# Performance work log

Measured on AMD Instinct MI355X. Metric: run time of the kernel, lower is better.

Reference implementation:

```python
import jax, jax.numpy as jnp
import numpy as np

INPUT_SIZE = 128
HIDDEN = 256
EPS = 1e-5  # PyTorch BatchNorm1d default


def setup_inputs() -> dict:
    key = jax.random.key(0)
    k1, k2, k3 = jax.random.split(key, 3)
    B, S = 128, 1024
    x = jax.random.normal(k1, (B, S, INPUT_SIZE), dtype=jnp.float32)
    fan_in = INPUT_SIZE + HIDDEN
    bound = 1.0 / np.sqrt(fan_in)
    # Linear(input+hidden -> 4*hidden); stored transposed for x @ W
    W = jax.random.uniform(k2, (fan_in, 4 * HIDDEN), minval=-bound, maxval=bound, dtype=jnp.float32)
    b = jax.random.uniform(k3, (4 * HIDDEN,), minval=-bound, maxval=bound, dtype=jnp.float32)
    gamma = jnp.ones((4, HIDDEN), dtype=jnp.float32)   # per-gate BN weight
    beta = jnp.zeros((4, HIDDEN), dtype=jnp.float32)   # per-gate BN bias
    return {"x": x, "W": W, "b": b, "gamma": gamma, "beta": beta}


def reference(x, W, b, gamma, beta):
    B, S, _ = x.shape
    H = HIDDEN

    def step(carry, x_t):
        hx, cx = carry
        g = jnp.concatenate([x_t, hx], axis=1) @ W + b          # [B, 4H]
        g = g.reshape(B, 4, H)
        # BatchNorm1d (training mode): batch statistics per gate/feature
        mean = g.mean(axis=0)                                   # [4, H]
        var = jnp.mean((g - mean) ** 2, axis=0)                 # biased var
        gn = (g - mean) * jax.lax.rsqrt(var + EPS) * gamma + beta
        i = jax.nn.sigmoid(gn[:, 0])
        f = jax.nn.sigmoid(gn[:, 1])
        c = jnp.tanh(gn[:, 2])
        o = jax.nn.sigmoid(gn[:, 3])
        cy = f * cx + i * c
        hy = o * jnp.tanh(cy)
        return (hy, cy), hy

    h0 = jnp.zeros((B, H), dtype=x.dtype)
    c0 = jnp.zeros((B, H), dtype=x.dtype)
    (hy, cy), outs = jax.lax.scan(step, (h0, c0), jnp.swapaxes(x, 0, 1))
    outputs = jnp.swapaxes(outs, 0, 1)                          # [B, S, H]
    return outputs, hy, cy
```

## Files before the change

kernel.cpp:

```cpp
#include <hip/hip_runtime.h>

#define BATCH 128
#define SEQ   1024
#define INSZ  128
#define HID   256
#define NBLK  32
#define NTHR  512
#define FPB   8
#define EPSV  1e-5f
#define SLAB  1032

typedef __attribute__((ext_vector_type(4))) float f32x4;
typedef __attribute__((ext_vector_type(8))) short short8;
typedef __attribute__((ext_vector_type(4))) unsigned u32x4;
typedef unsigned long long u64;
typedef unsigned u32;

__device__ __forceinline__ unsigned short f2bf(float f) {
  unsigned u = __builtin_bit_cast(unsigned, f);
  u += 0x7FFFu + ((u >> 16) & 1u);
  return (unsigned short)(u >> 16);
}
__device__ __forceinline__ short8 xcvt(float4 f0, float4 f1) {
  u32 a, b, c, d2;
  asm("v_cvt_pk_bf16_f32 %0, %1, %2" : "=v"(a)  : "v"(f0.x), "v"(f0.y));
  asm("v_cvt_pk_bf16_f32 %0, %1, %2" : "=v"(b)  : "v"(f0.z), "v"(f0.w));
  asm("v_cvt_pk_bf16_f32 %0, %1, %2" : "=v"(c)  : "v"(f1.x), "v"(f1.y));
  asm("v_cvt_pk_bf16_f32 %0, %1, %2" : "=v"(d2) : "v"(f1.z), "v"(f1.w));
  u32x4 t = {a, b, c, d2};
  return __builtin_bit_cast(short8, t);
}

__launch_bounds__(NTHR)
__global__ void bnlstm_kernel(const float* __restrict__ x,
                              const float* __restrict__ W,
                              const float* __restrict__ gamma,
                              const float* __restrict__ beta,
                              float* __restrict__ out,
                              unsigned short* __restrict__ hbuf,
                              u32* __restrict__ flags) {
  __shared__ __attribute__((aligned(16))) unsigned short Zs[32 * SLAB];
  __shared__ float red1[2][8][32];
  __shared__ float red2[2][8][32];
  __shared__ float waveTr[8][16][17];
  __shared__ __attribute__((aligned(16))) unsigned short hpack[8][16][8];

  const int tid   = threadIdx.x;
  const int bid   = blockIdx.x;
  const int lane  = tid & 63;
  const int wid   = tid >> 6;
  const int col16 = lane & 15;
  const int kg    = lane >> 4;
  const int d     = col16 & 3;
  const int q     = col16 >> 2;
  const int arow  = wid * 16 + col16;
  const int brow  = wid * 16 + kg * 4 + d;
  const int xb    = tid & 127;
  const int gb    = tid >> 7;

  short8 wf[2][12];
  for (int cg = 0; cg < 2; ++cg) {
    const int c32 = cg * 16 + col16;
    const int wcol = (c32 & 3) * HID + bid * FPB + (c32 >> 2);
    for (int kt = 0; kt < 12; ++kt) {
      short8 v;
      for (int e = 0; e < 8; ++e)
        v[e] = (short)f2bf(W[(kt * 32 + kg * 8 + e) * 1024 + wcol]);
      wf[cg][kt] = v;
    }
  }
  float gam = 0.f, bet = 0.f;
  if (lane < 32) {
    gam = gamma[(lane & 3) * HID + bid * FPB + (lane >> 2)];
    bet = beta [(lane & 3) * HID + bid * FPB + (lane >> 2)];
  }

  float cst[2] = {0.f, 0.f};
  float hnv[2];

  const float* xbase = x + (size_t)arow * (SEQ * INSZ) + kg * 8;
  float4 xv[8];
  #pragma unroll
  for (int kt = 0; kt < 4; ++kt) {
    xv[2 * kt]     = *(const float4*)(xbase + kt * 32);
    xv[2 * kt + 1] = *(const float4*)(xbase + kt * 32 + 4);
  }

  for (int t = 0; t < SEQ; ++t) {
    const int pR = t & 1;
    f32x4 acc0 = {0.f, 0.f, 0.f, 0.f}, acc1 = {0.f, 0.f, 0.f, 0.f};

    #pragma unroll
    for (int kt = 0; kt < 4; ++kt) {
      short8 ax = xcvt(xv[2 * kt], xv[2 * kt + 1]);
      acc0 = __builtin_amdgcn_mfma_f32_16x16x32_bf16(ax, wf[0][kt], acc0, 0, 0, 0);
      acc1 = __builtin_amdgcn_mfma_f32_16x16x32_bf16(ax, wf[1][kt], acc1, 0, 0, 0);
    }
    if (t + 1 < SEQ) {
      const float* xr = xbase + (size_t)(t + 1) * INSZ;
      #pragma unroll
      for (int kt = 0; kt < 4; ++kt) {
        xv[2 * kt]     = *(const float4*)(xr + kt * 32);
        xv[2 * kt + 1] = *(const float4*)(xr + kt * 32 + 4);
      }
    }

    if (t > 0) {
      if (wid == 0) {
        const u32 tv = (u32)t;
        while (true) {
          u32 v = (lane < NBLK)
            ? __hip_atomic_load(&flags[lane * 32], __ATOMIC_RELAXED, __HIP_MEMORY_SCOPE_AGENT)
            : tv;
          if (__all((int)(v >= tv))) break;
          __builtin_amdgcn_s_sleep(2);
        }
      }
      __syncthreads();

      const unsigned short* hsrc = hbuf + pR * (BATCH * HID);
      u32x4 hvv[8];
      #pragma unroll
      for (int k = 0; k < 8; ++k) {
        const unsigned short* ap = hsrc + ((gb + k * 4) * 128 + xb) * 8;
        asm volatile("global_load_dwordx4 %0, %1, off sc0 sc1"
                     : "=v"(hvv[k]) : "v"(ap));
      }
      asm volatile("s_waitcnt vmcnt(0)" ::: "memory");
      __builtin_amdgcn_sched_barrier(0);
      #pragma unroll
      for (int k = 0; k < 8; ++k)
        *(u32x4*)&Zs[(gb + k * 4) * SLAB + xb * 8] = hvv[k];
      __syncthreads();

      #pragma unroll
      for (int kt = 0; kt < 8; ++kt) {
        short8 af = *(const short8*)&Zs[(kt * 4 + kg) * SLAB + arow * 8];
        acc0 = __builtin_amdgcn_mfma_f32_16x16x32_bf16(af, wf[0][4 + kt], acc0, 0, 0, 0);
        acc1 = __builtin_amdgcn_mfma_f32_16x16x32_bf16(af, wf[1][4 + kt], acc1, 0, 0, 0);
      }
    }

    {
      float a1 = acc0[0] + acc0[1] + acc0[2] + acc0[3];
      float b1 = acc0[0]*acc0[0] + acc0[1]*acc0[1] + acc0[2]*acc0[2] + acc0[3]*acc0[3];
      float a2 = acc1[0] + acc1[1] + acc1[2] + acc1[3];
      float b2 = acc1[0]*acc1[0] + acc1[1]*acc1[1] + acc1[2]*acc1[2] + acc1[3]*acc1[3];
      a1 += __shfl_xor(a1, 16); b1 += __shfl_xor(b1, 16);
      a1 += __shfl_xor(a1, 32); b1 += __shfl_xor(b1, 32);
      a2 += __shfl_xor(a2, 16); b2 += __shfl_xor(b2, 16);
      a2 += __shfl_xor(a2, 32); b2 += __shfl_xor(b2, 32);
      if (lane < 16) {
        red1[pR][wid][lane] = a1;       red2[pR][wid][lane] = b1;
        red1[pR][wid][16 + lane] = a2;  red2[pR][wid][16 + lane] = b2;
      }
    }
    __syncthreads();

    float sc0v, sh0v, sc1v, sh1v;
    {
      const int cidx = lane & 31;
      float S1 = 0.f, S2 = 0.f;
      #pragma unroll
      for (int w2 = 0; w2 < 8; ++w2) { S1 += red1[pR][w2][cidx]; S2 += red2[pR][w2][cidx]; }
      float mean = S1 * (1.f / BATCH);
      float var  = fmaxf(S2 * (1.f / BATCH) - mean * mean, 0.f);
      float scl = rsqrtf(var + EPSV) * gam;
      float shl = bet - mean * scl;
      sc0v = __shfl(scl, col16);       sh0v = __shfl(shl, col16);
      sc1v = __shfl(scl, 16 + col16);  sh1v = __shfl(shl, 16 + col16);
    }

    #pragma unroll
    for (int cg = 0; cg < 2; ++cg) {
      f32x4 a = cg ? acc1 : acc0;
      const float sc = cg ? sc1v : sc0v, sh = cg ? sh1v : sh0v;
      #pragma unroll
      for (int i = 0; i < 4; ++i)
        waveTr[wid][kg * 4 + i][col16] = a[i] * sc + sh;
      float g0 = waveTr[wid][kg * 4 + d][q * 4 + 0];
      float g1 = waveTr[wid][kg * 4 + d][q * 4 + 1];
      float g2 = waveTr[wid][kg * 4 + d][q * 4 + 2];
      float g3 = waveTr[wid][kg * 4 + d][q * 4 + 3];
      float ig = 1.f / (1.f + __expf(-g0));
      float fg = 1.f / (1.f + __expf(-g1));
      float gg = 1.f - 2.f / (__expf(2.f * g2) + 1.f);
      float og = 1.f / (1.f + __expf(-g3));
      float cn = fg * cst[cg] + ig * gg;
      float hn = og * (1.f - 2.f / (__expf(2.f * cn) + 1.f));
      cst[cg] = cn;
      hnv[cg] = hn;
      hpack[wid][kg * 4 + d][cg * 4 + q] = f2bf(hn);
    }

    if (t < SEQ - 1) {
      if (lane < 16) {
        u32x4 hv = *(const u32x4*)&hpack[wid][lane][0];
        unsigned short* hd = hbuf + (pR ^ 1) * (BATCH * HID)
                           + (bid * 128 + wid * 16 + lane) * 8;
        asm volatile("global_store_dwordx4 %0, %1, off sc0 sc1"
                     :: "v"(hd), "v"(hv) : "memory");
      }
      asm volatile("s_waitcnt vmcnt(0)" ::: "memory");
      __syncthreads();
      if (tid == 0)
        __hip_atomic_store(&flags[bid * 32], (u32)(t + 1),
                           __ATOMIC_RELAXED, __HIP_MEMORY_SCOPE_AGENT);
      float* po = &out[(size_t)brow * (SEQ * HID) + (size_t)t * HID + bid * FPB];
      po[q]     = hnv[0];
      po[4 + q] = hnv[1];
    } else {
      float* po = &out[(size_t)brow * (SEQ * HID) + (size_t)t * HID + bid * FPB];
      po[q]     = hnv[0];
      po[4 + q] = hnv[1];
      float* ph = &out[(size_t)BATCH * SEQ * HID + (size_t)brow * HID + bid * FPB];
      ph[q] = hnv[0];                 ph[4 + q] = hnv[1];
      ph[BATCH * HID + q] = cst[0];   ph[BATCH * HID + 4 + q] = cst[1];
    }
  }
}

extern "C" void kernel_launch(void* const* d_in, const int* in_sizes, int n_in,
                              void* d_out, int out_size, void* d_ws, size_t ws_size,
                              hipStream_t stream) {
  const float* x     = (const float*)d_in[0];
  const float* W     = (const float*)d_in[1];
  const float* gamma = (const float*)d_in[3];
  const float* beta  = (const float*)d_in[4];
  float* out = (float*)d_out;

  u32* flags = (u32*)d_ws;
  unsigned short* hbuf = (unsigned short*)((char*)d_ws + 4096);

  (void)hipMemsetAsync(d_ws, 0, 4096, stream);
  hipLaunchKernelGGL(bnlstm_kernel, dim3(NBLK), dim3(NTHR), 0, stream,
                     x, W, gamma, beta, out, hbuf, flags);
}
```

Baseline: 5.269 ms.

## Halve persistent blocks to 16 with 1024 threads and stage Wx in LDS

Cuts the persistent grid from 32 to 16 blocks of 16 waves each, so each block owns 16 features and two wave groups split the 64 gate columns. This halves the number of blocks in the per-step cross-block flag barrier and h exchange. Input-weight fragments move from registers to LDS to free registers at the larger block size. The next-step x prefetch moves after the flag publish, and the spin sleep is shortened. The cost is more work per block on each step and more LDS traffic for the weight reads.

```diff
diff --git a/kernel.cpp b/kernel.cpp
--- a/kernel.cpp
+++ b/kernel.cpp
@@ -4,16 +4,15 @@
 #define SEQ   1024
 #define INSZ  128
 #define HID   256
-#define NBLK  32
-#define NTHR  512
-#define FPB   8
+#define NBLK  16
+#define NTHR  1024
+#define FPB   16
 #define EPSV  1e-5f
-#define SLAB  1032
+#define WXS   136
 
 typedef __attribute__((ext_vector_type(4))) float f32x4;
 typedef __attribute__((ext_vector_type(8))) short short8;
 typedef __attribute__((ext_vector_type(4))) unsigned u32x4;
-typedef unsigned long long u64;
 typedef unsigned u32;
 
 __device__ __forceinline__ unsigned short f2bf(float f) {
@@ -39,41 +38,53 @@
                               float* __restrict__ out,
                               unsigned short* __restrict__ hbuf,
                               u32* __restrict__ flags) {
-  __shared__ __attribute__((aligned(16))) unsigned short Zs[32 * SLAB];
-  __shared__ float red1[2][8][32];
-  __shared__ float red2[2][8][32];
-  __shared__ float waveTr[8][16][17];
-  __shared__ __attribute__((aligned(16))) unsigned short hpack[8][16][8];
+  __shared__ __attribute__((aligned(16))) unsigned short Zs[32 * 1024];
+  __shared__ __attribute__((aligned(16))) unsigned short Wx[64 * WXS];
+  __shared__ float red1[2][16][32];
+  __shared__ float red2[2][16][32];
+  __shared__ float waveTr[16][16][17];
+  __shared__ __attribute__((aligned(16))) unsigned short hpack[16][16][8];
 
   const int tid   = threadIdx.x;
   const int bid   = blockIdx.x;
   const int lane  = tid & 63;
   const int wid   = tid >> 6;
+  const int m     = wid & 7;
+  const int p     = wid >> 3;
   const int col16 = lane & 15;
   const int kg    = lane >> 4;
   const int d     = col16 & 3;
   const int q     = col16 >> 2;
-  const int arow  = wid * 16 + col16;
-  const int brow  = wid * 16 + kg * 4 + d;
-  const int xb    = tid & 127;
-  const int gb    = tid >> 7;
-
-  short8 wf[2][12];
-  for (int cg = 0; cg < 2; ++cg) {
-    const int c32 = cg * 16 + col16;
-    const int wcol = (c32 & 3) * HID + bid * FPB + (c32 >> 2);
-    for (int kt = 0; kt < 12; ++kt) {
+  const int arow  = m * 16 + col16;
+  const int brow  = m * 16 + kg * 4 + d;
+
+  {
+    const int c = tid >> 4, kb = (tid & 15) * 8;
+    const int wcol = (c & 3) * HID + bid * FPB + (c >> 2);
+    #pragma unroll
+    for (int e = 0; e < 8; ++e)
+      Wx[c * WXS + kb + e] = f2bf(W[(kb + e) * 1024 + wcol]);
+  }
+
+  short8 wf[2][8];
+  for (int cg2 = 0; cg2 < 2; ++cg2) {
+    const int c64 = p * 32 + cg2 * 16 + col16;
+    const int wcol = (c64 & 3) * HID + bid * FPB + (c64 >> 2);
+    for (int kth = 0; kth < 8; ++kth) {
       short8 v;
       for (int e = 0; e < 8; ++e)
-        v[e] = (short)f2bf(W[(kt * 32 + kg * 8 + e) * 1024 + wcol]);
-      wf[cg][kt] = v;
-    }
-  }
-  float gam = 0.f, bet = 0.f;
-  if (lane < 32) {
-    gam = gamma[(lane & 3) * HID + bid * FPB + (lane >> 2)];
-    bet = beta [(lane & 3) * HID + bid * FPB + (lane >> 2)];
-  }
+        v[e] = (short)f2bf(W[(128 + kth * 32 + kg * 8 + e) * 1024 + wcol]);
+      wf[cg2][kth] = v;
+    }
+  }
+  float gam, bet;
+  {
+    const int c64 = p * 32 + (lane & 31);
+    gam = gamma[(c64 & 3) * HID + bid * FPB + (c64 >> 2)];
+    bet = beta [(c64 & 3) * HID + bid * FPB + (c64 >> 2)];
+  }
+
+  __syncthreads();
 
   float cst[2] = {0.f, 0.f};
   float hnv[2];
@@ -93,16 +104,10 @@
     #pragma unroll
     for (int kt = 0; kt < 4; ++kt) {
       short8 ax = xcvt(xv[2 * kt], xv[2 * kt + 1]);
-      acc0 = __builtin_amdgcn_mfma_f32_16x16x32_bf16(ax, wf[0][kt], acc0, 0, 0, 0);
-      acc1 = __builtin_amdgcn_mfma_f32_16x16x32_bf16(ax, wf[1][kt], acc1, 0, 0, 0);
-    }
-    if (t + 1 < SEQ) {
-      const float* xr = xbase + (size_t)(t + 1) * INSZ;
-      #pragma unroll
-      for (int kt = 0; kt < 4; ++kt) {
-        xv[2 * kt]     = *(const float4*)(xr + kt * 32);
-        xv[2 * kt + 1] = *(const float4*)(xr + kt * 32 + 4);
-      }
+      short8 b0 = *(const short8*)&Wx[(p * 32 + col16) * WXS + kt * 32 + kg * 8];
+      short8 b1 = *(const short8*)&Wx[(p * 32 + 16 + col16) * WXS + kt * 32 + kg * 8];
+      acc0 = __builtin_amdgcn_mfma_f32_16x16x32_bf16(ax, b0, acc0, 0, 0, 0);
+      acc1 = __builtin_amdgcn_mfma_f32_16x16x32_bf16(ax, b1, acc1, 0, 0, 0);
     }
 
     if (t > 0) {
@@ -113,31 +118,34 @@
             ? __hip_atomic_load(&flags[lane * 32], __ATOMIC_RELAXED, __HIP_MEMORY_SCOPE_AGENT)
             : tv;
           if (__all((int)(v >= tv))) break;
-          __builtin_amdgcn_s_sleep(2);
+          __builtin_amdgcn_s_sleep(1);
         }
       }
       __syncthreads();
 
-      const unsigned short* hsrc = hbuf + pR * (BATCH * HID);
-      u32x4 hvv[8];
-      #pragma unroll
-      for (int k = 0; k < 8; ++k) {
-        const unsigned short* ap = hsrc + ((gb + k * 4) * 128 + xb) * 8;
+      const unsigned short* hsrc = hbuf + pR * 32768;
+      u32x4 hvv[4];
+      #pragma unroll
+      for (int k = 0; k < 4; ++k) {
+        const unsigned short* ap = hsrc + (tid + k * NTHR) * 8;
         asm volatile("global_load_dwordx4 %0, %1, off sc0 sc1"
                      : "=v"(hvv[k]) : "v"(ap));
       }
       asm volatile("s_waitcnt vmcnt(0)" ::: "memory");
       __builtin_amdgcn_sched_barrier(0);
       #pragma unroll
-      for (int k = 0; k < 8; ++k)
-        *(u32x4*)&Zs[(gb + k * 4) * SLAB + xb * 8] = hvv[k];
+      for (int k = 0; k < 4; ++k) {
+        const int idx = tid + k * NTHR;
+        const int s = idx >> 8, rem = idx & 255, r = rem >> 1, hh = rem & 1;
+        *(u32x4*)&Zs[(s * 2 + hh) * 1024 + r * 8] = hvv[k];
+      }
       __syncthreads();
 
       #pragma unroll
-      for (int kt = 0; kt < 8; ++kt) {
-        short8 af = *(const short8*)&Zs[(kt * 4 + kg) * SLAB + arow * 8];
-        acc0 = __builtin_amdgcn_mfma_f32_16x16x32_bf16(af, wf[0][4 + kt], acc0, 0, 0, 0);
-        acc1 = __builtin_amdgcn_mfma_f32_16x16x32_bf16(af, wf[1][4 + kt], acc1, 0, 0, 0);
+      for (int kth = 0; kth < 8; ++kth) {
+        short8 af = *(const short8*)&Zs[(kth * 4 + kg) * 1024 + arow * 8];
+        acc0 = __builtin_amdgcn_mfma_f32_16x16x32_bf16(af, wf[0][kth], acc0, 0, 0, 0);
+        acc1 = __builtin_amdgcn_mfma_f32_16x16x32_bf16(af, wf[1][kth], acc1, 0, 0, 0);
       }
     }
 
@@ -151,8 +159,8 @@
       a2 += __shfl_xor(a2, 16); b2 += __shfl_xor(b2, 16);
       a2 += __shfl_xor(a2, 32); b2 += __shfl_xor(b2, 32);
       if (lane < 16) {
-        red1[pR][wid][lane] = a1;       red2[pR][wid][lane] = b1;
-        red1[pR][wid][16 + lane] = a2;  red2[pR][wid][16 + lane] = b2;
+        red1[pR][wid][col16] = a1;       red2[pR][wid][col16] = b1;
+        red1[pR][wid][16 + col16] = a2;  red2[pR][wid][16 + col16] = b2;
       }
     }
     __syncthreads();
@@ -162,7 +170,10 @@
       const int cidx = lane & 31;
       float S1 = 0.f, S2 = 0.f;
       #pragma unroll
-      for (int w2 = 0; w2 < 8; ++w2) { S1 += red1[pR][w2][cidx]; S2 += red2[pR][w2][cidx]; }
+      for (int mm = 0; mm < 8; ++mm) {
+        S1 += red1[pR][(p << 3) | mm][cidx];
+        S2 += red2[pR][(p << 3) | mm][cidx];
+      }
       float mean = S1 * (1.f / BATCH);
       float var  = fmaxf(S2 * (1.f / BATCH) - mean * mean, 0.f);
       float scl = rsqrtf(var + EPSV) * gam;
@@ -172,9 +183,9 @@
     }
 
     #pragma unroll
-    for (int cg = 0; cg < 2; ++cg) {
-      f32x4 a = cg ? acc1 : acc0;
-      const float sc = cg ? sc1v : sc0v, sh = cg ? sh1v : sh0v;
+    for (int cg2 = 0; cg2 < 2; ++cg2) {
+      f32x4 a = cg2 ? acc1 : acc0;
+      const float sc = cg2 ? sc1v : sc0v, sh = cg2 ? sh1v : sh0v;
       #pragma unroll
       for (int i = 0; i < 4; ++i)
         waveTr[wid][kg * 4 + i][col16] = a[i] * sc + sh;
@@ -186,18 +197,18 @@
       float fg = 1.f / (1.f + __expf(-g1));
       float gg = 1.f - 2.f / (__expf(2.f * g2) + 1.f);
       float og = 1.f / (1.f + __expf(-g3));
-      float cn = fg * cst[cg] + ig * gg;
+      float cn = fg * cst[cg2] + ig * gg;
       float hn = og * (1.f - 2.f / (__expf(2.f * cn) + 1.f));
-      cst[cg] = cn;
-      hnv[cg] = hn;
-      hpack[wid][kg * 4 + d][cg * 4 + q] = f2bf(hn);
+      cst[cg2] = cn;
+      hnv[cg2] = hn;
+      hpack[wid][kg * 4 + d][cg2 * 4 + q] = f2bf(hn);
     }
 
     if (t < SEQ - 1) {
       if (lane < 16) {
         u32x4 hv = *(const u32x4*)&hpack[wid][lane][0];
-        unsigned short* hd = hbuf + (pR ^ 1) * (BATCH * HID)
-                           + (bid * 128 + wid * 16 + lane) * 8;
+        unsigned short* hd = hbuf + (pR ^ 1) * 32768
+                           + bid * 2048 + (m * 16 + lane) * 16 + p * 8;
         asm volatile("global_store_dwordx4 %0, %1, off sc0 sc1"
                      :: "v"(hd), "v"(hv) : "memory");
       }
@@ -206,14 +217,22 @@
       if (tid == 0)
         __hip_atomic_store(&flags[bid * 32], (u32)(t + 1),
                            __ATOMIC_RELAXED, __HIP_MEMORY_SCOPE_AGENT);
-      float* po = &out[(size_t)brow * (SEQ * HID) + (size_t)t * HID + bid * FPB];
+      {
+        float* po = &out[(size_t)brow * (SEQ * HID) + (size_t)t * HID + bid * FPB + p * 8];
+        po[q]     = hnv[0];
+        po[4 + q] = hnv[1];
+      }
+      const float* xr = xbase + (size_t)(t + 1) * INSZ;
+      #pragma unroll
+      for (int kt = 0; kt < 4; ++kt) {
+        xv[2 * kt]     = *(const float4*)(xr + kt * 32);
+        xv[2 * kt + 1] = *(const float4*)(xr + kt * 32 + 4);
+      }
+    } else {
+      float* po = &out[(size_t)brow * (SEQ * HID) + (size_t)t * HID + bid * FPB + p * 8];
       po[q]     = hnv[0];
       po[4 + q] = hnv[1];
-    } else {
-      float* po = &out[(size_t)brow * (SEQ * HID) + (size_t)t * HID + bid * FPB];
-      po[q]     = hnv[0];
-      po[4 + q] = hnv[1];
-      float* ph = &out[(size_t)BATCH * SEQ * HID + (size_t)brow * HID + bid * FPB];
+      float* ph = &out[(size_t)BATCH * SEQ * HID + (size_t)brow * HID + bid * FPB + p * 8];
       ph[q] = hnv[0];                 ph[4 + q] = hnv[1];
       ph[BATCH * HID + q] = cst[0];   ph[BATCH * HID + 4 + q] = cst[1];
     }
```

Result: slower. 12.47 ms (+136.7%).
